# Performance work log

Hardware: AMD Instinct MI355X
Metric: run time of the kernel (lower is better)

Reference implementation:

```python
import jax, jax.numpy as jnp
import numpy as np

N = 8192

def gcn_conv(x, edge_index, W, b):
    # PyG GCNConv: x' = D^{-1/2} (A + I) D^{-1/2} (x W) + b
    n = x.shape[0]
    loops = jnp.arange(n, dtype=edge_index.dtype)
    src = jnp.concatenate([edge_index[0], loops])
    dst = jnp.concatenate([edge_index[1], loops])
    h = x @ W  # transform first (as PyG does): [n, out]
    deg = jax.ops.segment_sum(jnp.ones_like(dst, dtype=h.dtype), dst, num_segments=n)
    dinv = jnp.where(deg > 0, jax.lax.rsqrt(deg), 0.0)
    norm = dinv[src] * dinv[dst]  # [E+n]
    out = jax.ops.segment_sum(norm[:, None] * h[src], dst, num_segments=n)
    return out + b


def setup_inputs() -> dict:
    key = jax.random.key(0)
    ks = jax.random.split(key, 9)
    F, H = 512, 512
    E = 262144
    x = jax.random.normal(ks[0], (N, F), dtype=jnp.float32)
    o = jax.random.normal(ks[1], (N, 4), dtype=jnp.float32)
    edge_index = jax.random.randint(ks[2], (2, E), 0, N, dtype=jnp.int64)
    s = 1.0 / np.sqrt(F)
    W1 = jax.random.uniform(ks[3], (F, H), jnp.float32, -s, s)
    b1 = jnp.zeros((H,), jnp.float32)
    s2 = 1.0 / np.sqrt(H)
    W2 = jax.random.uniform(ks[4], (H, 1), jnp.float32, -s2, s2)
    b2 = jnp.zeros((1,), jnp.float32)
    Wl = jax.random.uniform(ks[5], (4, 1), jnp.float32, -0.5, 0.5)
    bl = jnp.zeros((1,), jnp.float32)
    return {"x": x, "o": o, "edge_index": edge_index,
            "W1": W1, "b1": b1, "W2": W2, "b2": b2, "Wl": Wl, "bl": bl}


def reference(x, o, edge_index, W1, b1, W2, b2, Wl, bl):
    h = gcn_conv(x, edge_index, W1, b1)
    h = jax.nn.relu(h)
    h = gcn_conv(h, edge_index, W2, b2)  # [N, 1]
    h = h.mean(axis=1)                    # [N]
    ohe = o @ Wl + bl                      # [N, 1]
    # faithful to torch: [N] + [N,1] broadcasts to [N,N]
    return h + ohe
```

## Files before the change

### kernel.cpp

```cpp
#include <hip/hip_runtime.h>

#define NN 8192
#define FI 512
#define FH 512
#define RS 128

typedef __attribute__((ext_vector_type(8))) short short8;
typedef __attribute__((ext_vector_type(4))) float f32x4;
typedef __attribute__((ext_vector_type(2))) float f32x2;

__device__ __forceinline__ unsigned short f2bf(float f) {
    unsigned u = __float_as_uint(f);
    unsigned r = (u + 0x7fff + ((u >> 16) & 1)) >> 16;
    return (unsigned short)r;
}

#define GLOAD_LDS16(g, l)                                                        \
    __builtin_amdgcn_global_load_lds((__attribute__((address_space(1))) const void*)(g), \
                                     (__attribute__((address_space(3))) void*)(l), 16, 0, 0)

__global__ void k_zero(int* __restrict__ zero_base) {
    zero_base[blockIdx.x * 256 + threadIdx.x] = 0;
}

__global__ __launch_bounds__(256) void k_prepdeg(const float* __restrict__ x,
                                                 const float* __restrict__ W1,
                                                 const int* __restrict__ dstE, int E,
                                                 unsigned short* __restrict__ xb,
                                                 unsigned short* __restrict__ W1t,
                                                 int* __restrict__ deg) {
    int b = blockIdx.x, t = threadIdx.x;
    if (b < 1024) {
        #pragma unroll
        for (int u = 0; u < 4; ++u) {
            int i = (b * 4 + u) * 256 + t;
            float4 v = reinterpret_cast<const float4*>(x)[i];
            ushort4 h;
            h.x = f2bf(v.x); h.y = f2bf(v.y); h.z = f2bf(v.z); h.w = f2bf(v.w);
            reinterpret_cast<ushort4*>(xb)[i] = h;
        }
    } else if (b < 1088) {
        __shared__ float tile[64][65];
        int bi = (b - 1024) >> 3;
        int bj = (b - 1024) & 7;
        int c = t & 63, r0 = t >> 6;
        #pragma unroll
        for (int rr = 0; rr < 16; ++rr) {
            int row = rr * 4 + r0;
            tile[row][c] = W1[(size_t)(bi * 64 + row) * FH + bj * 64 + c];
        }
        __syncthreads();
        #pragma unroll
        for (int rr = 0; rr < 16; ++rr) {
            int row = rr * 4 + r0;
            W1t[(size_t)(bj * 64 + row) * FI + bi * 64 + c] = f2bf(tile[c][row]);
        }
    } else {
        int i = (b - 1088) * 256 + t;
        if (i < E) atomicAdd(&deg[dstE[i]], 1);
    }
}

__global__ __launch_bounds__(256) void k_fillgemm(const int* __restrict__ srcE,
                                                  const int* __restrict__ dstE, int E,
                                                  const int* __restrict__ deg,
                                                  int* __restrict__ cursor,
                                                  int2* __restrict__ csr,
                                                  const unsigned short* __restrict__ xb,
                                                  const unsigned short* __restrict__ W1t,
                                                  unsigned char* __restrict__ h8) {
    __shared__ __align__(16) unsigned short As[64 * 64];
    __shared__ __align__(16) unsigned short Bs[64 * 64];
    int bid = blockIdx.x, tid = threadIdx.x;

    if (bid < 1056) {
        int i = bid * 256 + tid;
        if (i < E) {
            int s = srcE[i], d = dstE[i];
            float w = rsqrtf((float)(deg[s] + 1)) * rsqrtf((float)(deg[d] + 1));
            int slot = atomicAdd(&cursor[d], 1);
            if (slot < RS) csr[(d << 7) + slot] = make_int2(s, __float_as_int(w));
        } else if (i < E + NN) {
            int v = i - E;
            float dv = rsqrtf((float)(deg[v] + 1));
            int slot = atomicAdd(&cursor[v], 1);
            if (slot < RS) csr[(v << 7) + slot] = make_int2(v, __float_as_int(dv * dv));
        }
        return;
    }

    int q0 = bid - 1056;
    int lane = tid & 63;
    int wave = tid >> 6;
    int wm = wave >> 1, wn = wave & 1;
    int bm = (q0 >> 3) * 64, bn = (q0 & 7) * 64;

    f32x4 acc[2][2] = {};
    int r  = lane & 15;
    int s0 = lane >> 4;

    for (int kt = 0; kt < FI / 64; ++kt) {
        #pragma unroll
        for (int t = 0; t < 2; ++t) {
            int q   = t * 256 + tid;
            int row = q >> 3;
            int sl  = q & 7;
            int sg  = sl ^ (row & 7);
            GLOAD_LDS16(xb  + (size_t)(bm + row) * FI + kt * 64 + sg * 8, As + q * 8);
            GLOAD_LDS16(W1t + (size_t)(bn + row) * FI + kt * 64 + sg * 8, Bs + q * 8);
        }
        __syncthreads();

        #pragma unroll
        for (int kc = 0; kc < 2; ++kc) {
            short8 a[2], b[2];
            #pragma unroll
            for (int m = 0; m < 2; ++m) {
                int row = wm * 32 + m * 16 + r;
                int sl  = (kc * 4 + s0) ^ (row & 7);
                a[m] = *reinterpret_cast<const short8*>(As + row * 64 + sl * 8);
            }
            #pragma unroll
            for (int n = 0; n < 2; ++n) {
                int row = wn * 32 + n * 16 + r;
                int sl  = (kc * 4 + s0) ^ (row & 7);
                b[n] = *reinterpret_cast<const short8*>(Bs + row * 64 + sl * 8);
            }
            #pragma unroll
            for (int m = 0; m < 2; ++m)
                #pragma unroll
                for (int n = 0; n < 2; ++n)
                    acc[m][n] = __builtin_amdgcn_mfma_f32_16x16x32_bf16(a[m], b[n], acc[m][n], 0, 0, 0);
        }
        __syncthreads();
    }

    #pragma unroll
    for (int m = 0; m < 2; ++m) {
        #pragma unroll
        for (int n = 0; n < 2; ++n) {
            int col = bn + wn * 32 + n * 16 + (lane & 15);
            int rw0 = bm + wm * 32 + m * 16 + (lane >> 4) * 4;
            #pragma unroll
            for (int reg = 0; reg < 4; ++reg) {
                float v = acc[m][n][reg];
                int pk = __builtin_amdgcn_cvt_pk_fp8_f32(v, v, 0, false);
                h8[(size_t)(rw0 + reg) * FH + col] = (unsigned char)(pk & 0xff);
            }
        }
    }
}

__device__ __forceinline__ void accp(f32x2* __restrict__ acc, uint2 rv, float w) {
    f32x2 wv = {w, w};
    acc[0] += wv * __builtin_amdgcn_cvt_pk_f32_fp8((int)rv.x, false);
    acc[1] += wv * __builtin_amdgcn_cvt_pk_f32_fp8((int)rv.x, true);
    acc[2] += wv * __builtin_amdgcn_cvt_pk_f32_fp8((int)rv.y, false);
    acc[3] += wv * __builtin_amdgcn_cvt_pk_f32_fp8((int)rv.y, true);
}

__global__ __launch_bounds__(256) void k_agg(const unsigned char* __restrict__ h8,
                                             const int* __restrict__ deg,
                                             const int2* __restrict__ csr,
                                             const float* __restrict__ b1,
                                             const float* __restrict__ W2,
                                             float* __restrict__ z) {
    int lane = threadIdx.x & 63;
    int v = blockIdx.x * 4 + (threadIdx.x >> 6);
    f32x2 acc[4] = {};
    int p0 = v << 7;
    int p1 = p0 + deg[v] + 1;
    for (int base = p0; base < p1; base += 64) {
        int cnt = p1 - base; if (cnt > 64) cnt = 64;
        int2 sw = (lane < cnt) ? csr[base + lane] : make_int2(0, 0);
        int j = 0;
        for (; j + 4 <= cnt; j += 4) {
            int   s0 = __shfl(sw.x, j),     s1 = __shfl(sw.x, j + 1);
            int   s2 = __shfl(sw.x, j + 2), s3 = __shfl(sw.x, j + 3);
            float w0 = __int_as_float(__shfl(sw.y, j));
            float w1 = __int_as_float(__shfl(sw.y, j + 1));
            float w2 = __int_as_float(__shfl(sw.y, j + 2));
            float w3 = __int_as_float(__shfl(sw.y, j + 3));
            uint2 r0 = *reinterpret_cast<const uint2*>(h8 + (size_t)s0 * FH + lane * 8);
            uint2 r1 = *reinterpret_cast<const uint2*>(h8 + (size_t)s1 * FH + lane * 8);
            uint2 r2 = *reinterpret_cast<const uint2*>(h8 + (size_t)s2 * FH + lane * 8);
            uint2 r3 = *reinterpret_cast<const uint2*>(h8 + (size_t)s3 * FH + lane * 8);
            accp(acc, r0, w0);
            accp(acc, r1, w1);
            accp(acc, r2, w2);
            accp(acc, r3, w3);
        }
        for (; j < cnt; ++j) {
            int   sj = __shfl(sw.x, j);
            float wj = __int_as_float(__shfl(sw.y, j));
            uint2 rj = *reinterpret_cast<const uint2*>(h8 + (size_t)sj * FH + lane * 8);
            accp(acc, rj, wj);
        }
    }
    const f32x2* b2p = reinterpret_cast<const f32x2*>(b1 + lane * 8);
    const f32x2* w2p = reinterpret_cast<const f32x2*>(W2 + lane * 8);
    float val = 0.f;
    #pragma unroll
    for (int q = 0; q < 4; ++q) {
        f32x2 t = acc[q] + b2p[q];
        t.x = fmaxf(t.x, 0.f);
        t.y = fmaxf(t.y, 0.f);
        f32x2 r = t * w2p[q];
        val += r.x + r.y;
    }
    #pragma unroll
    for (int off = 32; off; off >>= 1) val += __shfl_down(val, off);
    if (lane == 0) z[v] = val;
}

__global__ void k_node(const float* __restrict__ z,
                       const int* __restrict__ deg,
                       const int2* __restrict__ csr,
                       const float* __restrict__ b2,
                       const float* __restrict__ o,
                       const float* __restrict__ Wl,
                       const float* __restrict__ bl,
                       float* __restrict__ h2, float* __restrict__ ohe) {
    int v = blockIdx.x * blockDim.x + threadIdx.x;
    if (v >= NN) return;
    float acc = 0.f;
    int p0 = v << 7;
    int p1 = p0 + deg[v] + 1;
    for (int p = p0; p < p1; ++p) {
        int2 sw = csr[p];
        acc += __int_as_float(sw.y) * z[sw.x];
    }
    h2[v] = acc + b2[0];
    float4 ov = *reinterpret_cast<const float4*>(&o[(size_t)v * 4]);
    ohe[v] = ov.x * Wl[0] + ov.y * Wl[1] + ov.z * Wl[2] + ov.w * Wl[3] + bl[0];
}

__global__ __launch_bounds__(256) void k_out(const float* __restrict__ h2,
                                             const float* __restrict__ ohe,
                                             float4* __restrict__ out) {
    int i0 = blockIdx.x * 4;
    int t  = threadIdx.x;
    float4 h[8];
    #pragma unroll
    for (int u = 0; u < 8; ++u) h[u] = reinterpret_cast<const float4*>(h2)[u * 256 + t];
    #pragma unroll
    for (int rr = 0; rr < 4; ++rr) {
        float oi = ohe[i0 + rr];
        float4* dst = out + (size_t)(i0 + rr) * 2048;
        #pragma unroll
        for (int u = 0; u < 8; ++u) {
            float4 v = h[u];
            dst[u * 256 + t] = make_float4(v.x + oi, v.y + oi, v.z + oi, v.w + oi);
        }
    }
}

extern "C" void kernel_launch(void* const* d_in, const int* in_sizes, int n_in,
                              void* d_out, int out_size, void* d_ws, size_t ws_size,
                              hipStream_t stream) {
    const float* x  = (const float*)d_in[0];
    const float* o  = (const float*)d_in[1];
    const int*   ei = (const int*)d_in[2];
    const float* W1 = (const float*)d_in[3];
    const float* b1 = (const float*)d_in[4];
    const float* W2 = (const float*)d_in[5];
    const float* b2 = (const float*)d_in[6];
    const float* Wl = (const float*)d_in[7];
    const float* bl = (const float*)d_in[8];
    float* out = (float*)d_out;

    const int E = in_sizes[2] / 2;
    const int* src = ei;
    const int* dst = ei + E;

    char* p = (char*)d_ws;
    auto alloc = [&](size_t bytes) {
        char* r = p;
        p += (bytes + 255) & ~(size_t)255;
        return r;
    };
    int*   deg     = (int*)  alloc(NN * 4);
    int*   cursor  = (int*)  alloc(NN * 4);
    int2*  csr     = (int2*) alloc((size_t)NN * RS * 8);
    unsigned short* xb  = (unsigned short*)alloc((size_t)NN * FI * 2);
    unsigned short* W1t = (unsigned short*)alloc((size_t)FH * FI * 2);
    unsigned char*  h8  = (unsigned char*) alloc((size_t)NN * FH);
    float* z       = (float*)alloc(NN * 4);
    float* h2      = (float*)alloc(NN * 4);
    float* ohe     = (float*)alloc(NN * 4);

    k_zero    <<<64, 256, 0, stream>>>(deg);
    k_prepdeg <<<1088 + (E + 255) / 256, 256, 0, stream>>>(x, W1, dst, E, xb, W1t, deg);
    k_fillgemm<<<1056 + 1024, 256, 0, stream>>>(src, dst, E, deg, cursor, csr,
                                                xb, W1t, h8);
    k_agg     <<<NN / 4, 256, 0, stream>>>(h8, deg, csr, b1, W2, z);
    k_node    <<<(NN + 255) / 256, 256, 0, stream>>>(z, deg, csr, b2, o, Wl, bl, h2, ohe);
    k_out     <<<NN / 4, 256, 0, stream>>>(h2, ohe, (float4*)out);
}
```

Measured before the change: 124.9 us.

## Fuse second GCN layer into aggregation via transposed CSR scatter atomics

Removes the separate k_node kernel by building a transposed (source-major) CSR during the fill pass. After each node's layer-1 value is reduced, the kernel scatters weighted contributions to its destinations' h2 with float atomics. The ohe computation and the h2 bias init move into extra blocks of the prep kernel, and k_zero grows to clear the new cursor array. This saves one launch and a dependent gather pass, but doubles the CSR fill atomics and writes and adds float atomics, which also makes summation order nondeterministic.

```diff
diff --git a/kernel.cpp b/kernel.cpp
--- a/kernel.cpp
+++ b/kernel.cpp
@@ -26,10 +26,17 @@
 __global__ __launch_bounds__(256) void k_prepdeg(const float* __restrict__ x,
                                                  const float* __restrict__ W1,
                                                  const int* __restrict__ dstE, int E,
+                                                 const float* __restrict__ o,
+                                                 const float* __restrict__ Wl,
+                                                 const float* __restrict__ bl,
+                                                 const float* __restrict__ b2,
                                                  unsigned short* __restrict__ xb,
                                                  unsigned short* __restrict__ W1t,
-                                                 int* __restrict__ deg) {
+                                                 int* __restrict__ deg,
+                                                 float* __restrict__ ohe,
+                                                 float* __restrict__ h2) {
     int b = blockIdx.x, t = threadIdx.x;
+    int degB = (E + 255) >> 8;
     if (b < 1024) {
         #pragma unroll
         for (int u = 0; u < 4; ++u) {
@@ -55,9 +62,14 @@
             int row = rr * 4 + r0;
             W1t[(size_t)(bj * 64 + row) * FI + bi * 64 + c] = f2bf(tile[c][row]);
         }
-    } else {
+    } else if (b < 1088 + degB) {
         int i = (b - 1088) * 256 + t;
         if (i < E) atomicAdd(&deg[dstE[i]], 1);
+    } else {
+        int v = (b - 1088 - degB) * 256 + t;
+        float4 ov = *reinterpret_cast<const float4*>(&o[(size_t)v * 4]);
+        ohe[v] = ov.x * Wl[0] + ov.y * Wl[1] + ov.z * Wl[2] + ov.w * Wl[3] + bl[0];
+        h2[v] = b2[0];
     }
 }
 
@@ -65,7 +77,9 @@
                                                   const int* __restrict__ dstE, int E,
                                                   const int* __restrict__ deg,
                                                   int* __restrict__ cursor,
+                                                  int* __restrict__ cursorT,
                                                   int2* __restrict__ csr,
+                                                  int2* __restrict__ csrT,
                                                   const unsigned short* __restrict__ xb,
                                                   const unsigned short* __restrict__ W1t,
                                                   unsigned char* __restrict__ h8) {
@@ -78,13 +92,19 @@
         if (i < E) {
             int s = srcE[i], d = dstE[i];
             float w = rsqrtf((float)(deg[s] + 1)) * rsqrtf((float)(deg[d] + 1));
+            int wb = __float_as_int(w);
             int slot = atomicAdd(&cursor[d], 1);
-            if (slot < RS) csr[(d << 7) + slot] = make_int2(s, __float_as_int(w));
+            if (slot < RS) csr[(d << 7) + slot] = make_int2(s, wb);
+            int slotT = atomicAdd(&cursorT[s], 1);
+            if (slotT < RS) csrT[(s << 7) + slotT] = make_int2(d, wb);
         } else if (i < E + NN) {
             int v = i - E;
             float dv = rsqrtf((float)(deg[v] + 1));
+            int wb = __float_as_int(dv * dv);
             int slot = atomicAdd(&cursor[v], 1);
-            if (slot < RS) csr[(v << 7) + slot] = make_int2(v, __float_as_int(dv * dv));
+            if (slot < RS) csr[(v << 7) + slot] = make_int2(v, wb);
+            int slotT = atomicAdd(&cursorT[v], 1);
+            if (slotT < RS) csrT[(v << 7) + slotT] = make_int2(v, wb);
         }
         return;
     }
@@ -161,15 +181,18 @@
 
 __global__ __launch_bounds__(256) void k_agg(const unsigned char* __restrict__ h8,
                                              const int* __restrict__ deg,
+                                             const int* __restrict__ cursorT,
                                              const int2* __restrict__ csr,
+                                             const int2* __restrict__ csrT,
                                              const float* __restrict__ b1,
                                              const float* __restrict__ W2,
-                                             float* __restrict__ z) {
+                                             float* __restrict__ h2) {
     int lane = threadIdx.x & 63;
     int v = blockIdx.x * 4 + (threadIdx.x >> 6);
     f32x2 acc[4] = {};
     int p0 = v << 7;
-    int p1 = p0 + deg[v] + 1;
+    int cnt_all = deg[v] + 1; if (cnt_all > RS) cnt_all = RS;
+    int p1 = p0 + cnt_all;
     for (int base = p0; base < p1; base += 64) {
         int cnt = p1 - base; if (cnt > 64) cnt = 64;
         int2 sw = (lane < cnt) ? csr[base + lane] : make_int2(0, 0);
@@ -209,30 +232,13 @@
         val += r.x + r.y;
     }
     #pragma unroll
-    for (int off = 32; off; off >>= 1) val += __shfl_down(val, off);
-    if (lane == 0) z[v] = val;
-}
-
-__global__ void k_node(const float* __restrict__ z,
-                       const int* __restrict__ deg,
-                       const int2* __restrict__ csr,
-                       const float* __restrict__ b2,
-                       const float* __restrict__ o,
-                       const float* __restrict__ Wl,
-                       const float* __restrict__ bl,
-                       float* __restrict__ h2, float* __restrict__ ohe) {
-    int v = blockIdx.x * blockDim.x + threadIdx.x;
-    if (v >= NN) return;
-    float acc = 0.f;
-    int p0 = v << 7;
-    int p1 = p0 + deg[v] + 1;
-    for (int p = p0; p < p1; ++p) {
-        int2 sw = csr[p];
-        acc += __int_as_float(sw.y) * z[sw.x];
-    }
-    h2[v] = acc + b2[0];
-    float4 ov = *reinterpret_cast<const float4*>(&o[(size_t)v * 4]);
-    ohe[v] = ov.x * Wl[0] + ov.y * Wl[1] + ov.z * Wl[2] + ov.w * Wl[3] + bl[0];
+    for (int off = 32; off; off >>= 1) val += __shfl_xor(val, off);
+    int q0 = v << 7;
+    int cntT = cursorT[v]; if (cntT > RS) cntT = RS;
+    for (int p = q0 + lane; p < q0 + cntT; p += 64) {
+        int2 sw = csrT[p];
+        atomicAdd(&h2[sw.x], __int_as_float(sw.y) * val);
+    }
 }
 
 __global__ __launch_bounds__(256) void k_out(const float* __restrict__ h2,
@@ -272,6 +278,7 @@
     const int E = in_sizes[2] / 2;
     const int* src = ei;
     const int* dst = ei + E;
+    const int degB = (E + 255) >> 8;
 
     char* p = (char*)d_ws;
     auto alloc = [&](size_t bytes) {
@@ -281,19 +288,20 @@
     };
     int*   deg     = (int*)  alloc(NN * 4);
     int*   cursor  = (int*)  alloc(NN * 4);
+    int*   cursorT = (int*)  alloc(NN * 4);
     int2*  csr     = (int2*) alloc((size_t)NN * RS * 8);
+    int2*  csrT    = (int2*) alloc((size_t)NN * RS * 8);
     unsigned short* xb  = (unsigned short*)alloc((size_t)NN * FI * 2);
     unsigned short* W1t = (unsigned short*)alloc((size_t)FH * FI * 2);
     unsigned char*  h8  = (unsigned char*) alloc((size_t)NN * FH);
-    float* z       = (float*)alloc(NN * 4);
     float* h2      = (float*)alloc(NN * 4);
     float* ohe     = (float*)alloc(NN * 4);
 
-    k_zero    <<<64, 256, 0, stream>>>(deg);
-    k_prepdeg <<<1088 + (E + 255) / 256, 256, 0, stream>>>(x, W1, dst, E, xb, W1t, deg);
-    k_fillgemm<<<1056 + 1024, 256, 0, stream>>>(src, dst, E, deg, cursor, csr,
-                                                xb, W1t, h8);
-    k_agg     <<<NN / 4, 256, 0, stream>>>(h8, deg, csr, b1, W2, z);
-    k_node    <<<(NN + 255) / 256, 256, 0, stream>>>(z, deg, csr, b2, o, Wl, bl, h2, ohe);
+    k_zero    <<<96, 256, 0, stream>>>(deg);
+    k_prepdeg <<<1088 + degB + 32, 256, 0, stream>>>(x, W1, dst, E, o, Wl, bl, b2,
+                                                     xb, W1t, deg, ohe, h2);
+    k_fillgemm<<<1056 + 1024, 256, 0, stream>>>(src, dst, E, deg, cursor, cursorT,
+                                                csr, csrT, xb, W1t, h8);
+    k_agg     <<<NN / 4, 256, 0, stream>>>(h8, deg, cursorT, csr, csrT, b1, W2, h2);
     k_out     <<<NN / 4, 256, 0, stream>>>(h2, ohe, (float4*)out);
 }
```

Measured after the change: 128.2 us. +2.6%, slower.

## Fuse second-layer aggregation into output broadcast and move ohe into prep kernel

Applied to the files above, without the earlier changes.

Merges k_node and k_out into one kernel: each block recomputes 64 nodes' second-layer aggregation (4 threads per node), keeps them in shared memory, and writes a 256-row by 64-column tile of the N×N output. The ohe linear term moves into extra blocks of the prep kernel. This removes one launch and the h2 round trip, and parallelizes the per-node gather that was one thread per node. In exchange each node's aggregation is recomputed 32 times across blocks. Degree counts are now clamped to the CSR row stride.

```diff
diff --git a/kernel.cpp b/kernel.cpp
--- a/kernel.cpp
+++ b/kernel.cpp
@@ -26,10 +26,15 @@
 __global__ __launch_bounds__(256) void k_prepdeg(const float* __restrict__ x,
                                                  const float* __restrict__ W1,
                                                  const int* __restrict__ dstE, int E,
+                                                 const float* __restrict__ o,
+                                                 const float* __restrict__ Wl,
+                                                 const float* __restrict__ bl,
                                                  unsigned short* __restrict__ xb,
                                                  unsigned short* __restrict__ W1t,
-                                                 int* __restrict__ deg) {
+                                                 int* __restrict__ deg,
+                                                 float* __restrict__ ohe) {
     int b = blockIdx.x, t = threadIdx.x;
+    int degB = (E + 255) >> 8;
     if (b < 1024) {
         #pragma unroll
         for (int u = 0; u < 4; ++u) {
@@ -55,9 +60,13 @@
             int row = rr * 4 + r0;
             W1t[(size_t)(bj * 64 + row) * FI + bi * 64 + c] = f2bf(tile[c][row]);
         }
-    } else {
+    } else if (b < 1088 + degB) {
         int i = (b - 1088) * 256 + t;
         if (i < E) atomicAdd(&deg[dstE[i]], 1);
+    } else {
+        int v = (b - 1088 - degB) * 256 + t;
+        float4 ov = *reinterpret_cast<const float4*>(&o[(size_t)v * 4]);
+        ohe[v] = ov.x * Wl[0] + ov.y * Wl[1] + ov.z * Wl[2] + ov.w * Wl[3] + bl[0];
     }
 }
 
@@ -169,7 +178,8 @@
     int v = blockIdx.x * 4 + (threadIdx.x >> 6);
     f32x2 acc[4] = {};
     int p0 = v << 7;
-    int p1 = p0 + deg[v] + 1;
+    int cnt_all = deg[v] + 1; if (cnt_all > RS) cnt_all = RS;
+    int p1 = p0 + cnt_all;
     for (int base = p0; base < p1; base += 64) {
         int cnt = p1 - base; if (cnt > 64) cnt = 64;
         int2 sw = (lane < cnt) ? csr[base + lane] : make_int2(0, 0);
@@ -213,45 +223,43 @@
     if (lane == 0) z[v] = val;
 }
 
-__global__ void k_node(const float* __restrict__ z,
-                       const int* __restrict__ deg,
-                       const int2* __restrict__ csr,
-                       const float* __restrict__ b2,
-                       const float* __restrict__ o,
-                       const float* __restrict__ Wl,
-                       const float* __restrict__ bl,
-                       float* __restrict__ h2, float* __restrict__ ohe) {
-    int v = blockIdx.x * blockDim.x + threadIdx.x;
-    if (v >= NN) return;
-    float acc = 0.f;
-    int p0 = v << 7;
-    int p1 = p0 + deg[v] + 1;
-    for (int p = p0; p < p1; ++p) {
-        int2 sw = csr[p];
-        acc += __int_as_float(sw.y) * z[sw.x];
-    }
-    h2[v] = acc + b2[0];
-    float4 ov = *reinterpret_cast<const float4*>(&o[(size_t)v * 4]);
-    ohe[v] = ov.x * Wl[0] + ov.y * Wl[1] + ov.z * Wl[2] + ov.w * Wl[3] + bl[0];
-}
-
-__global__ __launch_bounds__(256) void k_out(const float* __restrict__ h2,
-                                             const float* __restrict__ ohe,
-                                             float4* __restrict__ out) {
-    int i0 = blockIdx.x * 4;
-    int t  = threadIdx.x;
-    float4 h[8];
+__global__ __launch_bounds__(256) void k_nodeout(const float* __restrict__ z,
+                                                 const int* __restrict__ deg,
+                                                 const int2* __restrict__ csr,
+                                                 const float* __restrict__ b2,
+                                                 const float* __restrict__ ohe,
+                                                 float4* __restrict__ out) {
+    __shared__ float h2s[64];
+    int s = blockIdx.x & 127;
+    int r = blockIdx.x >> 7;
+    int t = threadIdx.x;
+
+    {
+        int node = s * 64 + (t >> 2);
+        int q = t & 3;
+        int p0 = node << 7;
+        int cnt = deg[node] + 1; if (cnt > RS) cnt = RS;
+        float acc = 0.f;
+        for (int p = p0 + q; p < p0 + cnt; p += 4) {
+            int2 sw = csr[p];
+            acc += __int_as_float(sw.y) * z[sw.x];
+        }
+        acc += __shfl_down(acc, 1);
+        acc += __shfl_down(acc, 2);
+        if (q == 0) h2s[t >> 2] = acc + b2[0];
+    }
+    __syncthreads();
+
+    int rowLocal = t >> 4;
+    int colq     = t & 15;
+    float4 hv = reinterpret_cast<const float4*>(h2s)[colq];
+    int i0 = r * 256;
     #pragma unroll
-    for (int u = 0; u < 8; ++u) h[u] = reinterpret_cast<const float4*>(h2)[u * 256 + t];
-    #pragma unroll
-    for (int rr = 0; rr < 4; ++rr) {
-        float oi = ohe[i0 + rr];
-        float4* dst = out + (size_t)(i0 + rr) * 2048;
-        #pragma unroll
-        for (int u = 0; u < 8; ++u) {
-            float4 v = h[u];
-            dst[u * 256 + t] = make_float4(v.x + oi, v.y + oi, v.z + oi, v.w + oi);
-        }
+    for (int pass = 0; pass < 16; ++pass) {
+        int i = i0 + pass * 16 + rowLocal;
+        float oi = ohe[i];
+        out[(size_t)i * 2048 + s * 16 + colq] =
+            make_float4(hv.x + oi, hv.y + oi, hv.z + oi, hv.w + oi);
     }
 }
 
@@ -272,6 +280,7 @@
     const int E = in_sizes[2] / 2;
     const int* src = ei;
     const int* dst = ei + E;
+    const int degB = (E + 255) >> 8;
 
     char* p = (char*)d_ws;
     auto alloc = [&](size_t bytes) {
@@ -286,14 +295,13 @@
     unsigned short* W1t = (unsigned short*)alloc((size_t)FH * FI * 2);
     unsigned char*  h8  = (unsigned char*) alloc((size_t)NN * FH);
     float* z       = (float*)alloc(NN * 4);
-    float* h2      = (float*)alloc(NN * 4);
     float* ohe     = (float*)alloc(NN * 4);
 
     k_zero    <<<64, 256, 0, stream>>>(deg);
-    k_prepdeg <<<1088 + (E + 255) / 256, 256, 0, stream>>>(x, W1, dst, E, xb, W1t, deg);
+    k_prepdeg <<<1088 + degB + 32, 256, 0, stream>>>(x, W1, dst, E, o, Wl, bl,
+                                                     xb, W1t, deg, ohe);
     k_fillgemm<<<1056 + 1024, 256, 0, stream>>>(src, dst, E, deg, cursor, csr,
                                                 xb, W1t, h8);
     k_agg     <<<NN / 4, 256, 0, stream>>>(h8, deg, csr, b1, W2, z);
-    k_node    <<<(NN + 255) / 256, 256, 0, stream>>>(z, deg, csr, b2, o, Wl, bl, h2, ohe);
-    k_out     <<<NN / 4, 256, 0, stream>>>(h2, ohe, (float4*)out);
-}
+    k_nodeout <<<4096, 256, 0, stream>>>(z, deg, csr, b2, ohe, (float4*)out);
+}
```

After: 119.5 us. 4.3% less time.
